# Performance work log

Measured on AMD Instinct MI355X. Metric: run time of the kernel, lower is better.

## Reference

```python
import jax, jax.numpy as jnp
import numpy as np

BN_EPS = 1e-5
K_NEIGHBOR = 30
NUM_GRAPH = 4


def _bn_lrelu(x, g, b, axes):
    # BatchNorm in training mode (batch stats, biased var) + LeakyReLU(0.2).
    mean = jnp.mean(x, axes, keepdims=True)
    var = jnp.var(x, axes, keepdims=True)
    y = (x - mean) * jax.lax.rsqrt(var + BN_EPS) * g + b
    return jnp.where(y > 0, y, 0.2 * y)


def _pairwise_distance(pc):
    # pc: (B, N, C) -> (B, N, N) squared euclidean distances
    inner = -2.0 * jnp.einsum('bnc,bmc->bnm', pc, pc)
    sq = jnp.sum(pc * pc, axis=-1, keepdims=True)
    return sq + inner + jnp.swapaxes(sq, 1, 2)


def _knn(adj, k):
    return jax.lax.top_k(-adj, k)[1]  # (B, N, k)


def _edge_feature(pc, idx):
    # pc: (B, N, C), idx: (B, N, k) -> (B, N, k, 2C)
    B = pc.shape[0]
    nbrs = pc[jnp.arange(B)[:, None, None], idx]          # (B, N, k, C)
    central = jnp.broadcast_to(pc[:, :, None, :], nbrs.shape)
    return jnp.concatenate([central, nbrs - central], axis=-1)


def _forward(input_image, w64, g64, b64, w128, g128, b128, w1024, g1024, b1024,
             fc1_w, fc1_b, fc2_w, fc2_b, tw, tb,
             wo1, go1, bo1, wo2, go2, bo2, wo3, go3, bo3,
             w1, g1, b1, w2, g2, b2, w3, g3, b3):
    pc = jnp.transpose(input_image, (0, 2, 1))            # (B, N, 3)
    k = K_NEIGHBOR

    # ---- input transform net ----
    idx = _knn(_pairwise_distance(pc), k)
    ef = _edge_feature(pc, idx)                           # (B, N, k, 6)
    net = _bn_lrelu(ef @ w64.T, g64, b64, (0, 1, 2))      # (B, N, k, 64)
    net = _bn_lrelu(net @ w128.T, g128, b128, (0, 1, 2))  # (B, N, k, 128)
    net = jnp.max(net, axis=2)                            # (B, N, 128)
    net = _bn_lrelu(net @ w1024.T, g1024, b1024, (0, 1))  # (B, N, 1024)
    net = jnp.max(net, axis=1)                            # (B, 1024)
    net = net @ fc1_w.T + fc1_b
    net = net @ fc2_w.T + fc2_b                           # (B, 256)
    transform = net @ tw + (jnp.eye(3, dtype=jnp.float32).reshape(-1) + tb)
    transform = transform.reshape(-1, 3, 3)               # (B, 3, 3)

    pct = pc @ transform                                  # (B, N, 3)

    # ---- feature extraction on transformed cloud ----
    idx = _knn(_pairwise_distance(pct), k)
    ef = _edge_feature(pct, idx)                          # (B, N, k, 6)
    out1 = _bn_lrelu(ef @ wo1.T, go1, bo1, (0, 1, 2))     # (B, N, k, 64)
    out2 = _bn_lrelu(out1 @ wo2.T, go2, bo2, (0, 1, 2))   # (B, N, k, 64)
    nmax = jnp.max(out2, axis=2)
    nmean = jnp.mean(out2, axis=2)
    cat1 = jnp.concatenate([nmax, nmean], axis=-1)        # (B, N, 128)
    out3 = _bn_lrelu(cat1 @ wo3.T, go3, bo3, (0, 1))      # (B, N, 64)

    # ---- num_graph dynamic-graph blocks ----
    out5s, maxs, means = [], [], []
    for _ in range(NUM_GRAPH):
        IF = jnp.concatenate([pct, out3], axis=-1)        # (B, N, 67)
        trans1 = _bn_lrelu(IF @ w1.T, g1, b1, (0, 1))     # (B, N, 3)
        idx = _knn(_pairwise_distance(trans1), k)
        ef = _edge_feature(IF, idx)                       # (B, N, k, 134)
        out4 = _bn_lrelu(ef @ w2.T, g2, b2, (0, 1, 2))    # (B, N, k, 16)
        nm2 = jnp.max(out4, axis=2)                       # (B, N, 16)
        ne2 = jnp.mean(out4, axis=2)
        o5 = jnp.concatenate([nm2, ne2], axis=-1)         # (B, N, 32)
        out5 = _bn_lrelu(o5 @ w3.T, g3, b3, (0, 1))       # (B, N, 16)
        out5s.append(out5); maxs.append(nm2); means.append(ne2)

    def _pack(xs):
        x = jnp.concatenate(xs, axis=-1)                  # (B, N, 64)
        return jnp.transpose(x, (0, 2, 1))[..., None]     # (B, 64, N, 1)

    return (_pack(out5s), _pack(maxs), _pack(means))


def setup_inputs() -> dict:
    key = jax.random.key(0)
    ks = iter(jax.random.split(key, 64))
    def w(shape, s=0.05):
        return jax.random.normal(next(ks), shape, jnp.float32) * s
    B, N = 4, 2048
    inp = {'input_image': jax.random.normal(next(ks), (B, 3, N), jnp.float32)}
    for name, shp in [('w64', (64, 6)), ('w128', (128, 64)), ('w1024', (1024, 128)),
                      ('wo1', (64, 6)), ('wo2', (64, 64)), ('wo3', (64, 128)),
                      ('w1', (3, 67)), ('w2', (16, 134)), ('w3', (16, 32))]:
        inp[name] = w(shp)
        c = shp[0]
        inp['g' + name[1:]] = jnp.ones((c,), jnp.float32)
        inp['b' + name[1:]] = jnp.zeros((c,), jnp.float32)
    inp['fc1_w'] = w((512, 1024)); inp['fc1_b'] = jnp.zeros((512,), jnp.float32)
    inp['fc2_w'] = w((256, 512)); inp['fc2_b'] = jnp.zeros((256,), jnp.float32)
    inp['tw'] = w((256, 9)); inp['tb'] = w((9,))
    return inp


def reference(input_image, w64, g64, b64, w128, g128, b128, w1024, g1024, b1024,
              fc1_w, fc1_b, fc2_w, fc2_b, tw, tb,
              wo1, go1, bo1, wo2, go2, bo2, wo3, go3, bo3,
              w1, g1, b1, w2, g2, b2, w3, g3, b3):
    return _forward(input_image, w64, g64, b64, w128, g128, b128, w1024, g1024, b1024,
                    fc1_w, fc1_b, fc2_w, fc2_b, tw, tb,
                    wo1, go1, bo1, wo2, go2, bo2, wo3, go3, bo3,
                    w1, g1, b1, w2, g2, b2, w3, g3, b3)
```

## Files before the change

### kernel.cpp

```cpp
#include <hip/hip_runtime.h>


#define DEV __device__ __forceinline__
DEV float lrelu(float y) { return y > 0.f ? y : 0.2f * y; }
DEV unsigned fmap(float x) {
  unsigned u = __float_as_uint(x);
  return (u & 0x80000000u) ? ~u : (u | 0x80000000u);
}
DEV float funmap(unsigned m) {
  unsigned u = (m & 0x80000000u) ? (m & 0x7FFFFFFFu) : ~m;
  return __uint_as_float(u);
}

__global__ void zero_kernel(float* p, int n) {
  int id = blockIdx.x * 256 + threadIdx.x;
  if (id < n) p[id] = 0.f;
}

__global__ void iminit_kernel(unsigned* maxm, unsigned* minm) {
  int id = blockIdx.x * 256 + threadIdx.x;
  if (id < 4096) { maxm[id] = 0u; minm[id] = 0xFFFFFFFFu; }
}

__global__ void pc_kernel(const float* __restrict__ in, float* __restrict__ pc) {
  int id = blockIdx.x * 256 + threadIdx.x;
  if (id >= 4 * 3 * 2048) return;
  int n = id & 2047;
  int c = (id >> 11) % 3;
  int b = id / (3 * 2048);
  pc[((b << 11) + n) * 3 + c] = in[id];
}

__global__ __launch_bounds__(256) void knn_kernel(const float* __restrict__ pts, int* __restrict__ idx_out) {
  __shared__ double dist[4][2048];
  int tid = threadIdx.x;
  int w = tid >> 6, lane = tid & 63;
  int bn = (blockIdx.x << 2) + w;
  int b = bn >> 11;
  const float* base = pts + (b << 11) * 3;
  double qx = pts[bn * 3 + 0], qy = pts[bn * 3 + 1], qz = pts[bn * 3 + 2];
  double sqn = qx * qx + qy * qy + qz * qz;
  double* d = dist[w];
  double cmin = 1e300; int cpos = 0x7fffffff;
#pragma unroll 4
  for (int i = 0; i < 32; ++i) {
    int m = lane + (i << 6);
    double px = base[m * 3 + 0], py = base[m * 3 + 1], pz = base[m * 3 + 2];
    double v = sqn - 2.0 * (qx * px + qy * py + qz * pz) + (px * px + py * py + pz * pz);
    d[m] = v;
    if (v < cmin) { cmin = v; cpos = m; }
  }
  int* out = idx_out + bn * 30;
  for (int it = 0; it < 30; ++it) {
    double gv = cmin; int gp = cpos;
#pragma unroll
    for (int off = 1; off < 64; off <<= 1) {
      double ov = __shfl_xor(gv, off, 64);
      int op = __shfl_xor(gp, off, 64);
      if (ov < gv || (ov == gv && op < gp)) { gv = ov; gp = op; }
    }
    if (lane == 0) out[it] = gp;
    if (lane == (gp & 63)) {
      d[gp] = 1e300;
      cmin = 1e300; cpos = 0x7fffffff;
      for (int i = 0; i < 32; ++i) {
        int m = lane + (i << 6);
        double v = d[m];
        if (v < cmin) { cmin = v; cpos = m; }
      }
    }
  }
}

__global__ __launch_bounds__(256) void mom6_kernel(const float* __restrict__ pts, const int* __restrict__ idx,
                                                   double* __restrict__ acc) {
  __shared__ double sred[4][27];
  int tid = threadIdx.x;
  int lane = tid & 63, w = tid >> 6;
  double m[27];
#pragma unroll
  for (int i = 0; i < 27; ++i) m[i] = 0.0;
  int stride = gridDim.x << 8;
  for (int e = (blockIdx.x << 8) + tid; e < 245760; e += stride) {
    int bn = e / 30; int b = bn >> 11;
    int nb = idx[e];
    const float* cen = pts + bn * 3;
    const float* nbp = pts + ((b << 11) + nb) * 3;
    float f[6];
    f[0] = cen[0]; f[1] = cen[1]; f[2] = cen[2];
    f[3] = nbp[0] - f[0]; f[4] = nbp[1] - f[1]; f[5] = nbp[2] - f[2];
    int t = 6;
#pragma unroll
    for (int i = 0; i < 6; ++i) {
      m[i] += f[i];
#pragma unroll
      for (int j = i; j < 6; ++j) m[t++] += (double)f[i] * f[j];
    }
  }
#pragma unroll
  for (int i = 0; i < 27; ++i) {
    double v = m[i];
    v += __shfl_xor(v, 1, 64); v += __shfl_xor(v, 2, 64); v += __shfl_xor(v, 4, 64);
    v += __shfl_xor(v, 8, 64); v += __shfl_xor(v, 16, 64); v += __shfl_xor(v, 32, 64);
    m[i] = v;
  }
  if (lane == 0) {
#pragma unroll
    for (int i = 0; i < 27; ++i) sred[w][i] = m[i];
  }
  __syncthreads();
  if (tid < 27) atomicAdd(&acc[tid], sred[0][tid] + sred[1][tid] + sred[2][tid] + sred[3][tid]);
}

__global__ void finE1_kernel(const double* __restrict__ acc, const float* __restrict__ W,
                             const float* __restrict__ g, const float* __restrict__ bb,
                             float* __restrict__ sc) {
  int c = threadIdx.x;
  if (c >= 64) return;
  double wv[6];
#pragma unroll
  for (int i = 0; i < 6; ++i) wv[i] = W[c * 6 + i];
  double s = 0.0;
#pragma unroll
  for (int i = 0; i < 6; ++i) s += wv[i] * acc[i];
  double q = 0.0; int t = 6;
#pragma unroll
  for (int i = 0; i < 6; ++i)
#pragma unroll
    for (int j = i; j < 6; ++j) {
      double mm = acc[t++];
      q += (i == j) ? wv[i] * wv[i] * mm : 2.0 * wv[i] * wv[j] * mm;
    }
  const double E = 245760.0;
  double mean = s / E;
  double var = q / E - mean * mean;
  if (var < 0) var = 0;
  float sf = g[c] * (float)(1.0 / sqrt(var + 1e-5));
  sc[c] = sf;
  sc[64 + c] = bb[c] - (float)mean * sf;
}

template <int C2>
__global__ __launch_bounds__(256) void statsE_kernel(const float* __restrict__ pts, const int* __restrict__ idx,
                                                     const float* __restrict__ W1, const float* __restrict__ sc1,
                                                     const float* __restrict__ W2, double* __restrict__ acc) {
  __shared__ float xl[32 * 264];
  __shared__ double bacc[2 * C2];
  int tid = threadIdx.x;
  for (int i = tid; i < 2 * C2; i += 256) bacc[i] = 0.0;
  __syncthreads();
  int q8 = tid >> 3, l7 = tid & 7;
  for (int iter = 0; iter < 2; ++iter) {
    int e = iter * 122880 + (blockIdx.x << 8) + tid;
    int bn = e / 30;
    int b = bn >> 11;
    int nb = idx[e];
    const float* cen = pts + bn * 3;
    const float* nbp = pts + ((b << 11) + nb) * 3;
    float cx = cen[0], cy = cen[1], cz = cen[2];
    float dx = nbp[0] - cx, dy = nbp[1] - cy, dz = nbp[2] - cz;
    float y[64];
#pragma unroll
    for (int j = 0; j < 64; ++j) {
      float x = cx * W1[j * 6 + 0] + cy * W1[j * 6 + 1] + cz * W1[j * 6 + 2]
              + dx * W1[j * 6 + 3] + dy * W1[j * 6 + 4] + dz * W1[j * 6 + 5];
      y[j] = lrelu(fmaf(x, sc1[j], sc1[64 + j]));
    }
    for (int cc = 0; cc < C2 / 32; ++cc) {
      for (int q = 0; q < 32; ++q) {
        const float* w = W2 + (cc * 32 + q) * 64;
        float a0 = 0.f, a1 = 0.f, a2 = 0.f, a3 = 0.f;
#pragma unroll
        for (int j = 0; j < 64; j += 4) {
          a0 += y[j] * w[j]; a1 += y[j + 1] * w[j + 1];
          a2 += y[j + 2] * w[j + 2]; a3 += y[j + 3] * w[j + 3];
        }
        xl[q * 264 + tid] = (a0 + a1) + (a2 + a3);
      }
      __syncthreads();
      double sv = 0.0, qv = 0.0;
#pragma unroll 8
      for (int i = 0; i < 32; ++i) {
        float v = xl[q8 * 264 + l7 + (i << 3)];
        sv += v; qv += (double)v * v;
      }
      sv += __shfl_down(sv, 4, 8); sv += __shfl_down(sv, 2, 8); sv += __shfl_down(sv, 1, 8);
      qv += __shfl_down(qv, 4, 8); qv += __shfl_down(qv, 2, 8); qv += __shfl_down(qv, 1, 8);
      if (l7 == 0) { bacc[cc * 32 + q8] += sv; bacc[C2 + cc * 32 + q8] += qv; }
      __syncthreads();
    }
  }
  if (tid < 2 * C2) atomicAdd(&acc[tid], bacc[tid]);
}

__global__ __launch_bounds__(256) void poolA_kernel(const float* __restrict__ pts, const int* __restrict__ idx,
                                                    const float* __restrict__ W1, const float* __restrict__ sc1,
                                                    const float* __restrict__ W2, const float* __restrict__ sc2,
                                                    float* __restrict__ m128) {
  int tid = threadIdx.x;
  int lane = tid & 63;
  int k = lane & 31;
  int bn = (blockIdx.x << 3) + ((tid >> 6) << 1) + (lane >> 5);
  int b = bn >> 11;
  bool valid = k < 30;
  int nb = idx[bn * 30 + (valid ? k : 0)];
  const float* cen = pts + bn * 3;
  const float* nbp = pts + ((b << 11) + nb) * 3;
  float cx = cen[0], cy = cen[1], cz = cen[2];
  float dx = nbp[0] - cx, dy = nbp[1] - cy, dz = nbp[2] - cz;
  float y[64];
#pragma unroll
  for (int j = 0; j < 64; ++j) {
    float x = cx * W1[j * 6 + 0] + cy * W1[j * 6 + 1] + cz * W1[j * 6 + 2]
            + dx * W1[j * 6 + 3] + dy * W1[j * 6 + 4] + dz * W1[j * 6 + 5];
    y[j] = lrelu(fmaf(x, sc1[j], sc1[64 + j]));
  }
  for (int cc = 0; cc < 4; ++cc) {
    float kv = 0.f;
    for (int q = 0; q < 32; ++q) {
      int c = cc * 32 + q;
      const float* w = W2 + c * 64;
      float a0 = 0.f, a1 = 0.f, a2 = 0.f, a3 = 0.f;
#pragma unroll
      for (int j = 0; j < 64; j += 4) {
        a0 = fmaf(y[j], w[j], a0); a1 = fmaf(y[j + 1], w[j + 1], a1);
        a2 = fmaf(y[j + 2], w[j + 2], a2); a3 = fmaf(y[j + 3], w[j + 3], a3);
      }
      float v = lrelu(fmaf((a0 + a1) + (a2 + a3), sc2[c], sc2[128 + c]));
      v = valid ? v : -3.4e38f;
#pragma unroll
      for (int off = 1; off < 32; off <<= 1) v = fmaxf(v, __shfl_xor(v, off, 64));
      if (k == q) kv = v;
    }
    m128[bn * 128 + cc * 32 + k] = kv;
  }
}

__global__ __launch_bounds__(256) void poolB_kernel(const float* __restrict__ pts, const int* __restrict__ idx,
                                                    const float* __restrict__ W1, const float* __restrict__ sc1,
                                                    const float* __restrict__ W2, const float* __restrict__ sc2,
                                                    float* __restrict__ cat) {
  int tid = threadIdx.x;
  int lane = tid & 63;
  int k = lane & 31;
  int bn = (blockIdx.x << 3) + ((tid >> 6) << 1) + (lane >> 5);
  int b = bn >> 11;
  bool valid = k < 30;
  int nb = idx[bn * 30 + (valid ? k : 0)];
  const float* cen = pts + bn * 3;
  const float* nbp = pts + ((b << 11) + nb) * 3;
  float cx = cen[0], cy = cen[1], cz = cen[2];
  float dx = nbp[0] - cx, dy = nbp[1] - cy, dz = nbp[2] - cz;
  float y[64];
#pragma unroll
  for (int j = 0; j < 64; ++j) {
    float x = cx * W1[j * 6 + 0] + cy * W1[j * 6 + 1] + cz * W1[j * 6 + 2]
            + dx * W1[j * 6 + 3] + dy * W1[j * 6 + 4] + dz * W1[j * 6 + 5];
    y[j] = lrelu(fmaf(x, sc1[j], sc1[64 + j]));
  }
  for (int cc = 0; cc < 2; ++cc) {
    float kvm = 0.f, kvs = 0.f;
    for (int q = 0; q < 32; ++q) {
      int c = cc * 32 + q;
      const float* w = W2 + c * 64;
      float a0 = 0.f, a1 = 0.f, a2 = 0.f, a3 = 0.f;
#pragma unroll
      for (int j = 0; j < 64; j += 4) {
        a0 = fmaf(y[j], w[j], a0); a1 = fmaf(y[j + 1], w[j + 1], a1);
        a2 = fmaf(y[j + 2], w[j + 2], a2); a3 = fmaf(y[j + 3], w[j + 3], a3);
      }
      float v = lrelu(fmaf((a0 + a1) + (a2 + a3), sc2[c], sc2[64 + c]));
      float vm = valid ? v : -3.4e38f;
      float vs = valid ? v : 0.f;
#pragma unroll
      for (int off = 1; off < 32; off <<= 1) {
        vm = fmaxf(vm, __shfl_xor(vm, off, 64));
        vs += __shfl_xor(vs, off, 64);
      }
      if (k == q) { kvm = vm; kvs = vs; }
    }
    cat[bn * 128 + cc * 32 + k] = kvm;
    cat[bn * 128 + 64 + cc * 32 + k] = kvs * (1.f / 30.f);
  }
}

__global__ __launch_bounds__(256) void xo3g_kernel(const float* __restrict__ cat, const float* __restrict__ W3,
                                                   float* __restrict__ xo3T) {
  int tid = threadIdx.x;
  int lane = tid & 63, cw = tid >> 6;
  int bn = (blockIdx.x << 6) + lane;
  const float* cr = cat + bn * 128;
  float a[16];
#pragma unroll
  for (int q = 0; q < 16; ++q) a[q] = 0.f;
  for (int j = 0; j < 128; ++j) {
    float v = cr[j];
#pragma unroll
    for (int q = 0; q < 16; ++q) a[q] += v * W3[(cw * 16 + q) * 128 + j];
  }
#pragma unroll
  for (int q = 0; q < 16; ++q) xo3T[(cw * 16 + q) * 8192 + bn] = a[q];
}

__global__ __launch_bounds__(256) void rstats_kernel(const float* __restrict__ x, int E, int C,
                                                     double* __restrict__ acc) {
  __shared__ double rd[256];
  int c = blockIdx.x, tid = threadIdx.x;
  const float* r = x + (size_t)c * E;
  double ls = 0, lq = 0;
  for (int i = tid; i < E; i += 256) { float v = r[i]; ls += v; lq += (double)v * v; }
  rd[tid] = ls; __syncthreads();
  for (int s = 128; s > 0; s >>= 1) { if (tid < s) rd[tid] += rd[tid + s]; __syncthreads(); }
  if (tid == 0) acc[c] = rd[0];
  __syncthreads();
  rd[tid] = lq; __syncthreads();
  for (int s = 128; s > 0; s >>= 1) { if (tid < s) rd[tid] += rd[tid + s]; __syncthreads(); }
  if (tid == 0) acc[C + c] = rd[0];
}

__global__ __launch_bounds__(256) void cmm1024_kernel(const float* __restrict__ m128, const float* __restrict__ W,
                                                      double* __restrict__ acc, unsigned* __restrict__ maxm,
                                                      unsigned* __restrict__ minm) {
  __shared__ float mt[64 * 132];
  int tid = threadIdx.x;
  int lane = tid & 63;
  int b = blockIdx.x >> 8;
  int cg = (blockIdx.x >> 2) & 63;
  int ns = blockIdx.x & 3;
  int wu = __builtin_amdgcn_readfirstlane(tid >> 6);
  int cbase = cg * 16 + wu * 4;
  const float* wr = W + (size_t)cbase * 128;
  double ls[4] = {0, 0, 0, 0}, lq[4] = {0, 0, 0, 0};
  float mx[4], mn[4];
#pragma unroll
  for (int q = 0; q < 4; ++q) { mx[q] = -3.4e38f; mn[q] = 3.4e38f; }
  for (int ch = 0; ch < 8; ++ch) {
    int n0 = (ns << 9) + (ch << 6);
    __syncthreads();
    for (int i = tid; i < 2048; i += 256) {
      int r = i >> 5, jj = (i & 31) << 2;
      *(float4*)&mt[r * 132 + jj] = *(const float4*)&m128[(size_t)((b << 11) + n0 + r) * 128 + jj];
    }
    __syncthreads();
    float a[4] = {0.f, 0.f, 0.f, 0.f};
    const float* mrow = &mt[lane * 132];
#pragma unroll
    for (int j = 0; j < 128; j += 4) {
      float4 mv = *(const float4*)&mrow[j];
#pragma unroll
      for (int q = 0; q < 4; ++q) {
        const float* wq = wr + q * 128 + j;
        a[q] = fmaf(mv.x, wq[0], a[q]);
        a[q] = fmaf(mv.y, wq[1], a[q]);
        a[q] = fmaf(mv.z, wq[2], a[q]);
        a[q] = fmaf(mv.w, wq[3], a[q]);
      }
    }
#pragma unroll
    for (int q = 0; q < 4; ++q) {
      ls[q] += a[q]; lq[q] += (double)a[q] * a[q];
      mx[q] = fmaxf(mx[q], a[q]); mn[q] = fminf(mn[q], a[q]);
    }
  }
#pragma unroll
  for (int q = 0; q < 4; ++q) {
    double s = ls[q], sq = lq[q];
    float xm = mx[q], xn = mn[q];
    for (int off = 1; off < 64; off <<= 1) {
      s += __shfl_xor(s, off, 64);
      sq += __shfl_xor(sq, off, 64);
      xm = fmaxf(xm, __shfl_xor(xm, off, 64));
      xn = fminf(xn, __shfl_xor(xn, off, 64));
    }
    if (lane == 0) {
      int c = cbase + q;
      atomicAdd(&acc[c], s);
      atomicAdd(&acc[1024 + c], sq);
      atomicMax(&maxm[(b << 10) + c], fmap(xm));
      atomicMin(&minm[(b << 10) + c], fmap(xn));
    }
  }
}

__global__ void fin1024_kernel(const double* __restrict__ acc, const float* __restrict__ g,
                               const float* __restrict__ bb, const unsigned* __restrict__ maxm,
                               const unsigned* __restrict__ minm, float* __restrict__ gmax) {
  int c = blockIdx.x * 256 + threadIdx.x;
  if (c >= 1024) return;
  double mean = acc[c] / 8192.0;
  double var = acc[1024 + c] / 8192.0 - mean * mean;
  if (var < 0) var = 0;
  float s = g[c] * (float)(1.0 / sqrt(var + 1e-5));
  float t = bb[c] - (float)mean * s;
  for (int b = 0; b < 4; ++b) {
    float xm = (s >= 0.f) ? funmap(maxm[(b << 10) + c]) : funmap(minm[(b << 10) + c]);
    gmax[(b << 10) + c] = lrelu(fmaf(xm, s, t));
  }
}

__global__ __launch_bounds__(256) void fc_kernel(const float* __restrict__ gmax,
                                                 const float* __restrict__ fc1w, const float* __restrict__ fc1b,
                                                 const float* __restrict__ fc2w, const float* __restrict__ fc2b,
                                                 const float* __restrict__ tw, const float* __restrict__ tb,
                                                 float* __restrict__ transform) {
  __shared__ float net[1024];
  __shared__ float h1[512];
  __shared__ float h2[256];
  int b = blockIdx.x, tid = threadIdx.x;
  for (int i = tid; i < 1024; i += 256) net[i] = gmax[b * 1024 + i];
  __syncthreads();
  for (int o = tid; o < 512; o += 256) {
    float a = fc1b[o];
    const float* w = fc1w + o * 1024;
    for (int j = 0; j < 1024; ++j) a += net[j] * w[j];
    h1[o] = a;
  }
  __syncthreads();
  {
    int o = tid;
    float a = fc2b[o];
    const float* w = fc2w + o * 512;
    for (int j = 0; j < 512; ++j) a += h1[j] * w[j];
    h2[o] = a;
  }
  __syncthreads();
  if (tid < 9) {
    float a = 0.f;
    for (int i = 0; i < 256; ++i) a += h2[i] * tw[i * 9 + tid];
    float eye = (tid == 0 || tid == 4 || tid == 8) ? 1.f : 0.f;
    transform[b * 9 + tid] = a + eye + tb[tid];
  }
}

__global__ void pct_kernel(const float* __restrict__ pc, const float* __restrict__ T, float* __restrict__ pct) {
  int id = blockIdx.x * 256 + threadIdx.x;
  if (id >= 8192) return;
  int b = id >> 11;
  const float* t = T + b * 9;
  float x = pc[id * 3 + 0], y = pc[id * 3 + 1], z = pc[id * 3 + 2];
  pct[id * 3 + 0] = x * t[0] + y * t[3] + z * t[6];
  pct[id * 3 + 1] = x * t[1] + y * t[4] + z * t[7];
  pct[id * 3 + 2] = x * t[2] + y * t[5] + z * t[8];
}

__global__ __launch_bounds__(256) void dstats_kernel(const float* __restrict__ x, int total, int C,
                                                     double* __restrict__ acc) {
  __shared__ double dred[256];
  int tid = threadIdx.x;
  int c = tid % C;
  double ls = 0, lq = 0;
  int stride = gridDim.x << 8;
  for (int id = (blockIdx.x << 8) + tid; id < total; id += stride) {
    float v = x[id];
    ls += v; lq += (double)v * v;
  }
  dred[tid] = ls; __syncthreads();
  if (tid < C) { double v = 0; for (int i = tid; i < 256; i += C) v += dred[i]; atomicAdd(&acc[c], v); }
  __syncthreads();
  dred[tid] = lq; __syncthreads();
  if (tid < C) { double v = 0; for (int i = tid; i < 256; i += C) v += dred[i]; atomicAdd(&acc[C + c], v); }
}

__global__ __launch_bounds__(256) void stats3_kernel(const float* __restrict__ x, int total, double* __restrict__ acc) {
  __shared__ double dred[256];
  int tid = threadIdx.x;
  double ls[3] = {0, 0, 0}, lq[3] = {0, 0, 0};
  int stride = gridDim.x << 8;
  for (int id = (blockIdx.x << 8) + tid; id < total; id += stride) {
    float v = x[id];
    int c = id % 3;
    ls[c] += v; lq[c] += (double)v * v;
  }
  for (int cc = 0; cc < 3; ++cc) {
    __syncthreads();
    dred[tid] = ls[cc]; __syncthreads();
    for (int s = 128; s > 0; s >>= 1) { if (tid < s) dred[tid] += dred[tid + s]; __syncthreads(); }
    if (tid == 0) atomicAdd(&acc[cc], dred[0]);
    __syncthreads();
    dred[tid] = lq[cc]; __syncthreads();
    for (int s = 128; s > 0; s >>= 1) { if (tid < s) dred[tid] += dred[tid + s]; __syncthreads(); }
    if (tid == 0) atomicAdd(&acc[3 + cc], dred[0]);
  }
}

__global__ void fin_kernel(const double* __restrict__ acc, const float* __restrict__ g, const float* __restrict__ bb,
                           double cnt, int C, float* __restrict__ sc) {
  int c = blockIdx.x * 256 + threadIdx.x;
  if (c >= C) return;
  double mean = acc[c] / cnt;
  double var = acc[C + c] / cnt - mean * mean;
  if (var < 0) var = 0;
  float inv = (float)(1.0 / sqrt(var + 1e-5));
  float s = g[c] * inv;
  sc[c] = s;
  sc[C + c] = bb[c] - (float)mean * s;
}

__global__ void if_kernel(const float* __restrict__ pct, const float* __restrict__ xo3T, const float* __restrict__ sc3,
                          float* __restrict__ IF) {
  int id = blockIdx.x * 256 + threadIdx.x;
  if (id >= 8192 * 67) return;
  int bn = id / 67, j = id % 67;
  float v;
  if (j < 3) v = pct[bn * 3 + j];
  else { int c = j - 3; v = lrelu(fmaf(xo3T[c * 8192 + bn], sc3[c], sc3[64 + c])); }
  IF[id] = v;
}

__global__ void xt1_kernel(const float* __restrict__ IF, const float* __restrict__ W, float* __restrict__ xt1) {
  int id = blockIdx.x * 256 + threadIdx.x;
  if (id >= 8192 * 3) return;
  int bn = id / 3, c = id % 3;
  const float* f = IF + bn * 67;
  const float* w = W + c * 67;
  float a = 0.f;
  for (int j = 0; j < 67; ++j) a += f[j] * w[j];
  xt1[id] = a;
}

__global__ void t1_kernel(const float* __restrict__ xt1, const float* __restrict__ sc, float* __restrict__ trans1) {
  int id = blockIdx.x * 256 + threadIdx.x;
  if (id >= 24576) return;
  int c = id % 3;
  trans1[id] = lrelu(fmaf(xt1[id], sc[c], sc[3 + c]));
}

__global__ __launch_bounds__(256) void x2_kernel(const float* __restrict__ IF, const int* __restrict__ idx,
                                                 const float* __restrict__ W, float* __restrict__ x2,
                                                 double* __restrict__ acc) {
  __shared__ float WT[134 * 16];
  __shared__ double dred[256];
  int tid = threadIdx.x;
  for (int i = tid; i < 134 * 16; i += 256) { int c = i & 15, j = i >> 4; WT[j * 16 + c] = W[c * 134 + j]; }
  __syncthreads();
  int c = tid & 15;
  double ls = 0, lq = 0;
  const int total = 245760 * 16;
  int stride = gridDim.x << 8;
  for (int id = (blockIdx.x << 8) + tid; id < total; id += stride) {
    int p = id >> 4;
    int bn = p / 30; int b = bn >> 11;
    int nb = idx[p];
    const float* cen = IF + (size_t)bn * 67;
    const float* nbp = IF + (size_t)((b << 11) + nb) * 67;
    float a = 0.f;
    for (int j = 0; j < 67; ++j) {
      float cj = cen[j];
      a += cj * WT[j * 16 + c];
      a += (nbp[j] - cj) * WT[(67 + j) * 16 + c];
    }
    x2[id] = a;
    ls += a; lq += (double)a * a;
  }
  dred[tid] = ls; __syncthreads();
  if (tid < 16) { double v = 0; for (int i = tid; i < 256; i += 16) v += dred[i]; atomicAdd(&acc[tid], v); }
  __syncthreads();
  dred[tid] = lq; __syncthreads();
  if (tid < 16) { double v = 0; for (int i = tid; i < 256; i += 16) v += dred[i]; atomicAdd(&acc[16 + tid], v); }
}

__global__ __launch_bounds__(256) void k5_kernel(const float* __restrict__ x2, const float* __restrict__ sc2,
                                                 const float* __restrict__ W3, float* __restrict__ nm2,
                                                 float* __restrict__ ne2, float* __restrict__ x3) {
  __shared__ float W3T[32 * 16];
  __shared__ float o5[4][32];
  int tid = threadIdx.x;
  for (int i = tid; i < 512; i += 256) { int c = i & 15, j = i >> 4; W3T[j * 16 + c] = W3[c * 32 + j]; }
  __syncthreads();
  int lane = tid & 63, w = tid >> 6;
  int bn = blockIdx.x * 4 + w;
  int c = lane & 15, kq = lane >> 4;
  float s = sc2[c], t = sc2[16 + c];
  float lm = -3.4e38f, lsm = 0.f;
  const float* xp = x2 + (size_t)bn * 30 * 16;
  for (int k = kq; k < 30; k += 4) {
    float v = lrelu(fmaf(xp[k * 16 + c], s, t));
    lm = fmaxf(lm, v); lsm += v;
  }
  float lm2 = fmaxf(lm, __shfl_down(lm, 32, 64)); lm2 = fmaxf(lm2, __shfl_down(lm2, 16, 64));
  float ls2 = lsm + __shfl_down(lsm, 32, 64); ls2 = ls2 + __shfl_down(ls2, 16, 64);
  if (lane < 16) {
    float mean = ls2 / 30.f;
    nm2[bn * 16 + c] = lm2;
    ne2[bn * 16 + c] = mean;
    o5[w][c] = lm2; o5[w][16 + c] = mean;
  }
  __syncthreads();
  if (lane < 16) {
    float a = 0.f;
#pragma unroll
    for (int j = 0; j < 32; ++j) a += o5[w][j] * W3T[j * 16 + c];
    x3[bn * 16 + c] = a;
  }
}

__global__ void out_kernel(const float* __restrict__ x3, const float* __restrict__ sc3,
                           const float* __restrict__ nm2, const float* __restrict__ ne2,
                           float* __restrict__ out) {
  int id = blockIdx.x * 256 + threadIdx.x;
  if (id >= 4 * 16 * 2048) return;
  int n = id & 2047;
  int j = (id >> 11) & 15;
  int b = id >> 15;
  int bn = (b << 11) + n;
  float v5 = lrelu(fmaf(x3[bn * 16 + j], sc3[j], sc3[16 + j]));
  float vm = nm2[bn * 16 + j];
  float ve = ne2[bn * 16 + j];
#pragma unroll
  for (int g = 0; g < 4; ++g) {
    size_t base = (size_t)(b * 64 + g * 16 + j) * 2048 + n;
    out[base] = v5;
    out[524288 + base] = vm;
    out[1048576 + base] = ve;
  }
}

extern "C" void kernel_launch(void* const* d_in, const int* in_sizes, int n_in,
                              void* d_out, int out_size, void* d_ws, size_t ws_size,
                              hipStream_t stream) {
  (void)n_in; (void)out_size; (void)ws_size;
  const float* input_image = (const float*)d_in[0];
  bool dict = (in_sizes[10] == 384);
  int I_wo1, I_go1, I_bo1, I_wo2, I_go2, I_bo2, I_wo3, I_go3, I_bo3;
  int I_w1, I_g1, I_b1, I_w2, I_g2, I_b2, I_w3, I_g3, I_b3;
  int I_fc1w, I_fc1b, I_fc2w, I_fc2b, I_tw, I_tb;
  if (dict) {
    I_wo1 = 10; I_go1 = 11; I_bo1 = 12; I_wo2 = 13; I_go2 = 14; I_bo2 = 15;
    I_wo3 = 16; I_go3 = 17; I_bo3 = 18;
    I_w1 = 19; I_g1 = 20; I_b1 = 21; I_w2 = 22; I_g2 = 23; I_b2 = 24; I_w3 = 25; I_g3 = 26; I_b3 = 27;
    I_fc1w = 28; I_fc1b = 29; I_fc2w = 30; I_fc2b = 31; I_tw = 32; I_tb = 33;
  } else {
    I_fc1w = 10; I_fc1b = 11; I_fc2w = 12; I_fc2b = 13; I_tw = 14; I_tb = 15;
    I_wo1 = 16; I_go1 = 17; I_bo1 = 18; I_wo2 = 19; I_go2 = 20; I_bo2 = 21;
    I_wo3 = 22; I_go3 = 23; I_bo3 = 24;
    I_w1 = 25; I_g1 = 26; I_b1 = 27; I_w2 = 28; I_g2 = 29; I_b2 = 30; I_w3 = 31; I_g3 = 32; I_b3 = 33;
  }
#define FIN(i) ((const float*)d_in[i])
  float* ws = (float*)d_ws;
  float* pc      = ws;
  float* pct     = ws + 24576;
  float* trans1  = ws + 49152;
  int*   idx1    = (int*)(ws + 73728);
  int*   idx2    = (int*)(ws + 319488);
  int*   idx3    = (int*)(ws + 565248);
  float* m128b   = ws + 811008;
  float* catb    = ws + 1859584;
  unsigned* maxmapb = (unsigned*)(ws + 2908160);
  unsigned* minmapb = (unsigned*)(ws + 2912256);
  float* gmaxb   = ws + 10248192;
  float* transf  = ws + 10252288;
  float* xo3T    = ws + 10252352;
  float* IFb     = ws + 10776640;
  float* xt1b    = ws + 11325504;
  float* x2b     = ws + 11350080;
  float* nm2b    = ws + 15282240;
  float* ne2b    = ws + 15413312;
  float* x3b     = ws + 15544384;
  double* acc    = (double*)(ws + 15675456);
  float* sc      = ws + 15683648;
  const double CNT_E = 245760.0, CNT_P = 8192.0;
  const int A64 = 0, A128 = 128, A1024 = 384, AO1 = 2432, AO2 = 2560, AO3 = 2688, AT1 = 2816, A2 = 2822, A3 = 2854;

  zero_kernel<<<32, 256, 0, stream>>>((float*)acc, 8192);
  iminit_kernel<<<16, 256, 0, stream>>>(maxmapb, minmapb);
  pc_kernel<<<96, 256, 0, stream>>>(input_image, pc);
  knn_kernel<<<2048, 256, 0, stream>>>(pc, idx1);
  mom6_kernel<<<32, 256, 0, stream>>>(pc, idx1, acc + A64);
  finE1_kernel<<<1, 64, 0, stream>>>(acc + A64, FIN(1), FIN(2), FIN(3), sc + A64);
  statsE_kernel<128><<<480, 256, 0, stream>>>(pc, idx1, FIN(1), sc + A64, FIN(4), acc + A128);
  fin_kernel<<<1, 256, 0, stream>>>(acc + A128, FIN(5), FIN(6), CNT_E, 128, sc + A128);
  poolA_kernel<<<1024, 256, 0, stream>>>(pc, idx1, FIN(1), sc + A64, FIN(4), sc + A128, m128b);
  cmm1024_kernel<<<1024, 256, 0, stream>>>(m128b, FIN(7), acc + A1024, maxmapb, minmapb);
  fin1024_kernel<<<4, 256, 0, stream>>>(acc + A1024, FIN(8), FIN(9), maxmapb, minmapb, gmaxb);
  fc_kernel<<<4, 256, 0, stream>>>(gmaxb, FIN(I_fc1w), FIN(I_fc1b), FIN(I_fc2w), FIN(I_fc2b), FIN(I_tw), FIN(I_tb), transf);
  pct_kernel<<<32, 256, 0, stream>>>(pc, transf, pct);
  knn_kernel<<<2048, 256, 0, stream>>>(pct, idx2);
  mom6_kernel<<<32, 256, 0, stream>>>(pct, idx2, acc + AO1);
  finE1_kernel<<<1, 64, 0, stream>>>(acc + AO1, FIN(I_wo1), FIN(I_go1), FIN(I_bo1), sc + AO1);
  statsE_kernel<64><<<480, 256, 0, stream>>>(pct, idx2, FIN(I_wo1), sc + AO1, FIN(I_wo2), acc + AO2);
  fin_kernel<<<1, 256, 0, stream>>>(acc + AO2, FIN(I_go2), FIN(I_bo2), CNT_E, 64, sc + AO2);
  poolB_kernel<<<1024, 256, 0, stream>>>(pct, idx2, FIN(I_wo1), sc + AO1, FIN(I_wo2), sc + AO2, catb);
  xo3g_kernel<<<128, 256, 0, stream>>>(catb, FIN(I_wo3), xo3T);
  rstats_kernel<<<64, 256, 0, stream>>>(xo3T, 8192, 64, acc + AO3);
  fin_kernel<<<1, 256, 0, stream>>>(acc + AO3, FIN(I_go3), FIN(I_bo3), CNT_P, 64, sc + AO3);
  if_kernel<<<2144, 256, 0, stream>>>(pct, xo3T, sc + AO3, IFb);
  xt1_kernel<<<96, 256, 0, stream>>>(IFb, FIN(I_w1), xt1b);
  stats3_kernel<<<32, 256, 0, stream>>>(xt1b, 24576, acc + AT1);
  fin_kernel<<<1, 256, 0, stream>>>(acc + AT1, FIN(I_g1), FIN(I_b1), CNT_P, 3, sc + AT1);
  t1_kernel<<<96, 256, 0, stream>>>(xt1b, sc + AT1, trans1);
  knn_kernel<<<2048, 256, 0, stream>>>(trans1, idx3);
  x2_kernel<<<512, 256, 0, stream>>>(IFb, idx3, FIN(I_w2), x2b, acc + A2);
  fin_kernel<<<1, 256, 0, stream>>>(acc + A2, FIN(I_g2), FIN(I_b2), CNT_E, 16, sc + A2);
  k5_kernel<<<2048, 256, 0, stream>>>(x2b, sc + A2, FIN(I_w3), nm2b, ne2b, x3b);
  dstats_kernel<<<256, 256, 0, stream>>>(x3b, 131072, 16, acc + A3);
  fin_kernel<<<1, 256, 0, stream>>>(acc + A3, FIN(I_g3), FIN(I_b3), CNT_P, 16, sc + A3);
  out_kernel<<<512, 256, 0, stream>>>(x3b, sc + A3, nm2b, ne2b, (float*)d_out);
#undef FIN
}
```

Measured before the change: 1.432 ms.

## Fuse edge conv stats with max/min pooling and keep kNN distances in registers

```diff
diff --git a/kernel.cpp b/kernel.cpp
--- a/kernel.cpp
+++ b/kernel.cpp
@@ -32,7 +32,6 @@
 }
 
 __global__ __launch_bounds__(256) void knn_kernel(const float* __restrict__ pts, int* __restrict__ idx_out) {
-  __shared__ double dist[4][2048];
   int tid = threadIdx.x;
   int w = tid >> 6, lane = tid & 63;
   int bn = (blockIdx.x << 2) + w;
@@ -40,16 +39,17 @@
   const float* base = pts + (b << 11) * 3;
   double qx = pts[bn * 3 + 0], qy = pts[bn * 3 + 1], qz = pts[bn * 3 + 2];
   double sqn = qx * qx + qy * qy + qz * qz;
-  double* d = dist[w];
+  double d[32];
   double cmin = 1e300; int cpos = 0x7fffffff;
-#pragma unroll 4
+#pragma unroll
   for (int i = 0; i < 32; ++i) {
     int m = lane + (i << 6);
     double px = base[m * 3 + 0], py = base[m * 3 + 1], pz = base[m * 3 + 2];
     double v = sqn - 2.0 * (qx * px + qy * py + qz * pz) + (px * px + py * py + pz * pz);
-    d[m] = v;
+    d[i] = v;
     if (v < cmin) { cmin = v; cpos = m; }
   }
+  unsigned rmask = 0u;
   int* out = idx_out + bn * 30;
   for (int it = 0; it < 30; ++it) {
     double gv = cmin; int gp = cpos;
@@ -61,12 +61,12 @@
     }
     if (lane == 0) out[it] = gp;
     if (lane == (gp & 63)) {
-      d[gp] = 1e300;
+      rmask |= 1u << (gp >> 6);
       cmin = 1e300; cpos = 0x7fffffff;
+#pragma unroll
       for (int i = 0; i < 32; ++i) {
-        int m = lane + (i << 6);
-        double v = d[m];
-        if (v < cmin) { cmin = v; cpos = m; }
+        double v = ((rmask >> i) & 1u) ? 1e300 : d[i];
+        if (v < cmin) { cmin = v; cpos = lane + (i << 6); }
       }
     }
   }
@@ -140,67 +140,17 @@
   sc[64 + c] = bb[c] - (float)mean * sf;
 }
 
-template <int C2>
-__global__ __launch_bounds__(256) void statsE_kernel(const float* __restrict__ pts, const int* __restrict__ idx,
-                                                     const float* __restrict__ W1, const float* __restrict__ sc1,
-                                                     const float* __restrict__ W2, double* __restrict__ acc) {
-  __shared__ float xl[32 * 264];
-  __shared__ double bacc[2 * C2];
-  int tid = threadIdx.x;
-  for (int i = tid; i < 2 * C2; i += 256) bacc[i] = 0.0;
-  __syncthreads();
-  int q8 = tid >> 3, l7 = tid & 7;
-  for (int iter = 0; iter < 2; ++iter) {
-    int e = iter * 122880 + (blockIdx.x << 8) + tid;
-    int bn = e / 30;
-    int b = bn >> 11;
-    int nb = idx[e];
-    const float* cen = pts + bn * 3;
-    const float* nbp = pts + ((b << 11) + nb) * 3;
-    float cx = cen[0], cy = cen[1], cz = cen[2];
-    float dx = nbp[0] - cx, dy = nbp[1] - cy, dz = nbp[2] - cz;
-    float y[64];
-#pragma unroll
-    for (int j = 0; j < 64; ++j) {
-      float x = cx * W1[j * 6 + 0] + cy * W1[j * 6 + 1] + cz * W1[j * 6 + 2]
-              + dx * W1[j * 6 + 3] + dy * W1[j * 6 + 4] + dz * W1[j * 6 + 5];
-      y[j] = lrelu(fmaf(x, sc1[j], sc1[64 + j]));
-    }
-    for (int cc = 0; cc < C2 / 32; ++cc) {
-      for (int q = 0; q < 32; ++q) {
-        const float* w = W2 + (cc * 32 + q) * 64;
-        float a0 = 0.f, a1 = 0.f, a2 = 0.f, a3 = 0.f;
-#pragma unroll
-        for (int j = 0; j < 64; j += 4) {
-          a0 += y[j] * w[j]; a1 += y[j + 1] * w[j + 1];
-          a2 += y[j + 2] * w[j + 2]; a3 += y[j + 3] * w[j + 3];
-        }
-        xl[q * 264 + tid] = (a0 + a1) + (a2 + a3);
-      }
-      __syncthreads();
-      double sv = 0.0, qv = 0.0;
-#pragma unroll 8
-      for (int i = 0; i < 32; ++i) {
-        float v = xl[q8 * 264 + l7 + (i << 3)];
-        sv += v; qv += (double)v * v;
-      }
-      sv += __shfl_down(sv, 4, 8); sv += __shfl_down(sv, 2, 8); sv += __shfl_down(sv, 1, 8);
-      qv += __shfl_down(qv, 4, 8); qv += __shfl_down(qv, 2, 8); qv += __shfl_down(qv, 1, 8);
-      if (l7 == 0) { bacc[cc * 32 + q8] += sv; bacc[C2 + cc * 32 + q8] += qv; }
-      __syncthreads();
-    }
-  }
-  if (tid < 2 * C2) atomicAdd(&acc[tid], bacc[tid]);
-}
-
-__global__ __launch_bounds__(256) void poolA_kernel(const float* __restrict__ pts, const int* __restrict__ idx,
+__global__ __launch_bounds__(256) void edgeA_kernel(const float* __restrict__ pts, const int* __restrict__ idx,
                                                     const float* __restrict__ W1, const float* __restrict__ sc1,
-                                                    const float* __restrict__ W2, const float* __restrict__ sc2,
-                                                    float* __restrict__ m128) {
+                                                    const float* __restrict__ W2,
+                                                    float* __restrict__ mxout, float* __restrict__ mnout,
+                                                    double* __restrict__ acc) {
+  __shared__ double sred[4][64][4];
   int tid = threadIdx.x;
   int lane = tid & 63;
+  int wv = tid >> 6;
   int k = lane & 31;
-  int bn = (blockIdx.x << 3) + ((tid >> 6) << 1) + (lane >> 5);
+  int bn = (blockIdx.x << 3) + (wv << 1) + (lane >> 5);
   int b = bn >> 11;
   bool valid = k < 30;
   int nb = idx[bn * 30 + (valid ? k : 0)];
@@ -215,8 +165,9 @@
             + dx * W1[j * 6 + 3] + dy * W1[j * 6 + 4] + dz * W1[j * 6 + 5];
     y[j] = lrelu(fmaf(x, sc1[j], sc1[64 + j]));
   }
+  double aS0 = 0.0, aQ0 = 0.0, aS1 = 0.0, aQ1 = 0.0;
   for (int cc = 0; cc < 4; ++cc) {
-    float kv = 0.f;
+    float kvx = 0.f, kvn = 0.f;
     for (int q = 0; q < 32; ++q) {
       int c = cc * 32 + q;
       const float* w = W2 + c * 64;
@@ -226,13 +177,101 @@
         a0 = fmaf(y[j], w[j], a0); a1 = fmaf(y[j + 1], w[j + 1], a1);
         a2 = fmaf(y[j + 2], w[j + 2], a2); a3 = fmaf(y[j + 3], w[j + 3], a3);
       }
-      float v = lrelu(fmaf((a0 + a1) + (a2 + a3), sc2[c], sc2[128 + c]));
-      v = valid ? v : -3.4e38f;
-#pragma unroll
-      for (int off = 1; off < 32; off <<= 1) v = fmaxf(v, __shfl_xor(v, off, 64));
-      if (k == q) kv = v;
-    }
-    m128[bn * 128 + cc * 32 + k] = kv;
+      float v = (a0 + a1) + (a2 + a3);
+      float vx = valid ? v : -3.4e38f;
+      float vn = valid ? v : 3.4e38f;
+      float sv = valid ? v : 0.f;
+      float sq = valid ? v * v : 0.f;
+#pragma unroll
+      for (int off = 1; off < 32; off <<= 1) {
+        vx = fmaxf(vx, __shfl_xor(vx, off, 64));
+        vn = fminf(vn, __shfl_xor(vn, off, 64));
+        sv += __shfl_xor(sv, off, 64);
+        sq += __shfl_xor(sq, off, 64);
+      }
+      sv += __shfl_xor(sv, 32, 64);
+      sq += __shfl_xor(sq, 32, 64);
+      if (k == q) { kvx = vx; kvn = vn; }
+      int ol = ((cc & 1) << 5) + q;
+      bool own = (lane == ol);
+      if (cc < 2) { aS0 += own ? (double)sv : 0.0; aQ0 += own ? (double)sq : 0.0; }
+      else        { aS1 += own ? (double)sv : 0.0; aQ1 += own ? (double)sq : 0.0; }
+    }
+    mxout[bn * 128 + cc * 32 + k] = kvx;
+    mnout[bn * 128 + cc * 32 + k] = kvn;
+  }
+  sred[wv][lane][0] = aS0; sred[wv][lane][1] = aQ0;
+  sred[wv][lane][2] = aS1; sred[wv][lane][3] = aQ1;
+  __syncthreads();
+  int l = tid >> 2, j = tid & 3;
+  double t = sred[0][l][j] + sred[1][l][j] + sred[2][l][j] + sred[3][l][j];
+  int ch = (j < 2) ? l : 64 + l;
+  atomicAdd(&acc[(j & 1) * 128 + ch], t);
+}
+
+__global__ void applyA_kernel(const float* __restrict__ mx, const float* __restrict__ mn,
+                              const float* __restrict__ sc, float* __restrict__ m128) {
+  int id = blockIdx.x * 256 + threadIdx.x;
+  if (id >= 8192 * 128) return;
+  int c = id & 127;
+  float s = sc[c], t = sc[128 + c];
+  float sel = (s >= 0.f) ? mx[id] : mn[id];
+  m128[id] = lrelu(fmaf(sel, s, t));
+}
+
+__global__ __launch_bounds__(256) void statsB_kernel(const float* __restrict__ pts, const int* __restrict__ idx,
+                                                     const float* __restrict__ W1, const float* __restrict__ sc1,
+                                                     const float* __restrict__ W2, double* __restrict__ acc) {
+  __shared__ double sred[4][64][2];
+  int tid = threadIdx.x;
+  int lane = tid & 63;
+  int wv = tid >> 6;
+  int k = lane & 31;
+  int bn = (blockIdx.x << 3) + (wv << 1) + (lane >> 5);
+  int b = bn >> 11;
+  bool valid = k < 30;
+  int nb = idx[bn * 30 + (valid ? k : 0)];
+  const float* cen = pts + bn * 3;
+  const float* nbp = pts + ((b << 11) + nb) * 3;
+  float cx = cen[0], cy = cen[1], cz = cen[2];
+  float dx = nbp[0] - cx, dy = nbp[1] - cy, dz = nbp[2] - cz;
+  float y[64];
+#pragma unroll
+  for (int j = 0; j < 64; ++j) {
+    float x = cx * W1[j * 6 + 0] + cy * W1[j * 6 + 1] + cz * W1[j * 6 + 2]
+            + dx * W1[j * 6 + 3] + dy * W1[j * 6 + 4] + dz * W1[j * 6 + 5];
+    y[j] = lrelu(fmaf(x, sc1[j], sc1[64 + j]));
+  }
+  double aS = 0.0, aQ = 0.0;
+  for (int cc = 0; cc < 2; ++cc) {
+    for (int q = 0; q < 32; ++q) {
+      int c = cc * 32 + q;
+      const float* w = W2 + c * 64;
+      float a0 = 0.f, a1 = 0.f, a2 = 0.f, a3 = 0.f;
+#pragma unroll
+      for (int j = 0; j < 64; j += 4) {
+        a0 = fmaf(y[j], w[j], a0); a1 = fmaf(y[j + 1], w[j + 1], a1);
+        a2 = fmaf(y[j + 2], w[j + 2], a2); a3 = fmaf(y[j + 3], w[j + 3], a3);
+      }
+      float v = (a0 + a1) + (a2 + a3);
+      float sv = valid ? v : 0.f;
+      float sq = valid ? v * v : 0.f;
+#pragma unroll
+      for (int off = 1; off < 64; off <<= 1) {
+        sv += __shfl_xor(sv, off, 64);
+        sq += __shfl_xor(sq, off, 64);
+      }
+      bool own = (lane == c);
+      aS += own ? (double)sv : 0.0;
+      aQ += own ? (double)sq : 0.0;
+    }
+  }
+  sred[wv][lane][0] = aS; sred[wv][lane][1] = aQ;
+  __syncthreads();
+  if (tid < 128) {
+    int l = tid >> 1, j = tid & 1;
+    double t = sred[0][l][j] + sred[1][l][j] + sred[2][l][j] + sred[3][l][j];
+    atomicAdd(&acc[j * 64 + l], t);
   }
 }
 
@@ -647,6 +686,8 @@
   float* catb    = ws + 1859584;
   unsigned* maxmapb = (unsigned*)(ws + 2908160);
   unsigned* minmapb = (unsigned*)(ws + 2912256);
+  float* m128mx  = ws + 2916352;
+  float* m128mn  = ws + 3964928;
   float* gmaxb   = ws + 10248192;
   float* transf  = ws + 10252288;
   float* xo3T    = ws + 10252352;
@@ -667,9 +708,9 @@
   knn_kernel<<<2048, 256, 0, stream>>>(pc, idx1);
   mom6_kernel<<<32, 256, 0, stream>>>(pc, idx1, acc + A64);
   finE1_kernel<<<1, 64, 0, stream>>>(acc + A64, FIN(1), FIN(2), FIN(3), sc + A64);
-  statsE_kernel<128><<<480, 256, 0, stream>>>(pc, idx1, FIN(1), sc + A64, FIN(4), acc + A128);
+  edgeA_kernel<<<1024, 256, 0, stream>>>(pc, idx1, FIN(1), sc + A64, FIN(4), m128mx, m128mn, acc + A128);
   fin_kernel<<<1, 256, 0, stream>>>(acc + A128, FIN(5), FIN(6), CNT_E, 128, sc + A128);
-  poolA_kernel<<<1024, 256, 0, stream>>>(pc, idx1, FIN(1), sc + A64, FIN(4), sc + A128, m128b);
+  applyA_kernel<<<4096, 256, 0, stream>>>(m128mx, m128mn, sc + A128, m128b);
   cmm1024_kernel<<<1024, 256, 0, stream>>>(m128b, FIN(7), acc + A1024, maxmapb, minmapb);
   fin1024_kernel<<<4, 256, 0, stream>>>(acc + A1024, FIN(8), FIN(9), maxmapb, minmapb, gmaxb);
   fc_kernel<<<4, 256, 0, stream>>>(gmaxb, FIN(I_fc1w), FIN(I_fc1b), FIN(I_fc2w), FIN(I_fc2b), FIN(I_tw), FIN(I_tb), transf);
@@ -677,7 +718,7 @@
   knn_kernel<<<2048, 256, 0, stream>>>(pct, idx2);
   mom6_kernel<<<32, 256, 0, stream>>>(pct, idx2, acc + AO1);
   finE1_kernel<<<1, 64, 0, stream>>>(acc + AO1, FIN(I_wo1), FIN(I_go1), FIN(I_bo1), sc + AO1);
-  statsE_kernel<64><<<480, 256, 0, stream>>>(pct, idx2, FIN(I_wo1), sc + AO1, FIN(I_wo2), acc + AO2);
+  statsB_kernel<<<1024, 256, 0, stream>>>(pct, idx2, FIN(I_wo1), sc + AO1, FIN(I_wo2), acc + AO2);
   fin_kernel<<<1, 256, 0, stream>>>(acc + AO2, FIN(I_go2), FIN(I_bo2), CNT_E, 64, sc + AO2);
   poolB_kernel<<<1024, 256, 0, stream>>>(pct, idx2, FIN(I_wo1), sc + AO1, FIN(I_wo2), sc + AO2, catb);
   xo3g_kernel<<<128, 256, 0, stream>>>(catb, FIN(I_wo3), xo3T);
```

Result: faster. 1.288 ms (-10.1%).
